# Kernel optimization log

Measured on AMD Instinct MI355X. Metric: run time of the kernel, lower is better.

## Reference

```python
import jax, jax.numpy as jnp
import numpy as np

B, T, D_LAT = 128, 256, 256
N_HIDDEN = 1024
H_SMALL = N_HIDDEN // 2  # 512: lstm1/lstm2 hidden size
H_BIG = N_HIDDEN         # 1024: lstm3 hidden size


def _p(key, shape, scale=0.05):
    return (jax.random.normal(key, shape, dtype=jnp.float32) * scale)


def setup_inputs() -> dict:
    key = jax.random.key(0)
    ks = jax.random.split(key, 16)
    return {
        "X": jax.random.normal(ks[0], (B, T, D_LAT), dtype=jnp.float32),
        # LSTMCell 1: input D_LAT -> hidden H_SMALL (torch layout: [4H, in])
        "W_ih1": _p(ks[1], (4 * H_SMALL, D_LAT)),
        "W_hh1": _p(ks[2], (4 * H_SMALL, H_SMALL)),
        "b_ih1": _p(ks[3], (4 * H_SMALL,)),
        "b_hh1": _p(ks[4], (4 * H_SMALL,)),
        # LSTMCell 2: H_SMALL -> H_SMALL
        "W_ih2": _p(ks[5], (4 * H_SMALL, H_SMALL)),
        "W_hh2": _p(ks[6], (4 * H_SMALL, H_SMALL)),
        "b_ih2": _p(ks[7], (4 * H_SMALL,)),
        "b_hh2": _p(ks[8], (4 * H_SMALL,)),
        # LSTMCell 3: H_SMALL -> H_BIG
        "W_ih3": _p(ks[9], (4 * H_BIG, H_SMALL)),
        "W_hh3": _p(ks[10], (4 * H_BIG, H_BIG)),
        "b_ih3": _p(ks[11], (4 * H_BIG,)),
        "b_hh3": _p(ks[12], (4 * H_BIG,)),
        # Linear: H_BIG -> D_LAT (torch layout: [out, in])
        "W_lin": _p(ks[13], (D_LAT, H_BIG)),
        "b_lin": _p(ks[14], (D_LAT,)),
    }


def _lstm_cell(x, h, c, W_ih, W_hh, b_ih, b_hh):
    # torch.nn.LSTMCell gate order: i, f, g, o
    gates = x @ W_ih.T + b_ih + h @ W_hh.T + b_hh  # [B, 4H]
    i, f, g, o = jnp.split(gates, 4, axis=-1)
    c_new = jax.nn.sigmoid(f) * c + jax.nn.sigmoid(i) * jnp.tanh(g)
    h_new = jax.nn.sigmoid(o) * jnp.tanh(c_new)
    return h_new, c_new


def reference(X, W_ih1, W_hh1, b_ih1, b_hh1,
              W_ih2, W_hh2, b_ih2, b_hh2,
              W_ih3, W_hh3, b_ih3, b_hh3,
              W_lin, b_lin):
    n = X.shape[0]
    z_s = jnp.zeros((n, H_SMALL), dtype=X.dtype)
    z_b = jnp.zeros((n, H_BIG), dtype=X.dtype)
    init = (z_s, z_s, z_s, z_s, z_b, z_b)

    def step(carry, x_t):
        h1, c1, h2, c2, h3, c3 = carry
        h1, c1 = _lstm_cell(x_t, h1, c1, W_ih1, W_hh1, b_ih1, b_hh1)
        h2, c2 = _lstm_cell(h1, h2, c2, W_ih2, W_hh2, b_ih2, b_hh2)
        h3, c3 = _lstm_cell(h2, h3, c3, W_ih3, W_hh3, b_ih3, b_hh3)
        out = h3 @ W_lin.T + b_lin  # [B, D_LAT]
        return (h1, c1, h2, c2, h3, c3), out

    xs = jnp.swapaxes(X, 0, 1)  # [T, B, D_LAT]
    _, outputs = jax.lax.scan(step, init, xs)
    return outputs  # [T, B, D_LAT] == torch.stack(outputs) with future=0
```

## Files before the change

### kernel.cpp

```cpp
#include <hip/hip_runtime.h>
#include <stdint.h>

#define NWG 208
#define NPHASE 259

typedef __attribute__((ext_vector_type(8))) short short8;
typedef __attribute__((ext_vector_type(4))) float floatx4;
typedef __attribute__((ext_vector_type(4))) unsigned int uintx4;

static constexpr int Bb = 128, Tt = 256, Dl = 256, Hs = 512, Hb = 1024;

static constexpr size_t OFF_FLAGS = 0;
static constexpr size_t OFF_B1  = 1024;
static constexpr size_t OFF_B2  = OFF_B1 + 2048*4;
static constexpr size_t OFF_B3  = OFF_B2 + 2048*4;
static constexpr size_t OFF_BL  = OFF_B3 + 4096*4;
static constexpr size_t OFF_W1  = OFF_BL + 1024;
static constexpr size_t OFF_W2  = OFF_W1 + (size_t)2048*768*2;
static constexpr size_t OFF_W3  = OFF_W2 + (size_t)2048*1024*2;
static constexpr size_t OFF_WL  = OFF_W3 + (size_t)4096*1536*2;
static constexpr size_t FIXED_END = OFF_WL + (size_t)256*1024*2;

template<int D> struct Lay {
  static constexpr size_t H1  = FIXED_END;
  static constexpr size_t H2  = H1 + (size_t)D*Bb*Hs*2;
  static constexpr size_t H3  = H2 + (size_t)D*Bb*Hs*2;
  static constexpr size_t XB  = H3 + (size_t)D*Bb*Hb*2;
  static constexpr size_t END = XB + (size_t)D*Bb*Dl*2;
};

static constexpr int SMEM_BYTES = 135168;
static constexpr int STG_OFF    = 131072;

__device__ __forceinline__ unsigned short f2bf(float f) {
  unsigned int u = __float_as_uint(f);
  unsigned int r = (u + 0x7fffu + ((u >> 16) & 1u)) >> 16;
  return (unsigned short)r;
}
__device__ __forceinline__ float sigm(float x) { return 1.f/(1.f + __expf(-x)); }
__device__ __forceinline__ float tanh_f(float x) {
  x = fminf(fmaxf(x, -15.f), 15.f);
  float e = __expf(-2.f*x);
  return (1.f - e)/(1.f + e);
}
__device__ __forceinline__ size_t blk_off(int row, int u) {
  return ((size_t)(u >> 5)*8 + (row >> 4))*512 + (size_t)((u & 31) >> 3)*128
       + (size_t)(row & 15)*8 + (u & 7);
}
__device__ __forceinline__ void st_dword_cg(void* p, unsigned int v) {
  asm volatile("global_store_dword %0, %1, off sc0 sc1" :: "v"(p), "v"(v) : "memory");
}
__device__ __forceinline__ void st_b128_cg(void* p, uintx4 v) {
  asm volatile("global_store_dwordx4 %0, %1, off sc0 sc1" :: "v"(p), "v"(v) : "memory");
}
__device__ __forceinline__ void waitcnt_vm0() {
  asm volatile("s_waitcnt vmcnt(0)" ::: "memory");
}

template<int D>
__global__ void lstm_init(
    const float* __restrict__ X,
    const float* __restrict__ Wih1, const float* __restrict__ Whh1,
    const float* __restrict__ bih1, const float* __restrict__ bhh1,
    const float* __restrict__ Wih2, const float* __restrict__ Whh2,
    const float* __restrict__ bih2, const float* __restrict__ bhh2,
    const float* __restrict__ Wih3, const float* __restrict__ Whh3,
    const float* __restrict__ bih3, const float* __restrict__ bhh3,
    const float* __restrict__ Wlin, const float* __restrict__ blin,
    unsigned char* __restrict__ ws)
{
  size_t i0 = (size_t)blockIdx.x*blockDim.x + threadIdx.x;
  size_t np = (size_t)gridDim.x*blockDim.x;

  unsigned int* fl = (unsigned int*)(ws + OFF_FLAGS);
  for (size_t i = i0; i < 256; i += np) fl[i] = (i < NWG) ? 0u : 0xFFFFFFFFu;

  float* b1 = (float*)(ws + OFF_B1);
  float* b2 = (float*)(ws + OFF_B2);
  float* b3 = (float*)(ws + OFF_B3);
  float* bl = (float*)(ws + OFF_BL);
  for (size_t i = i0; i < 2048; i += np) b1[i] = bih1[i] + bhh1[i];
  for (size_t i = i0; i < 2048; i += np) b2[i] = bih2[i] + bhh2[i];
  for (size_t i = i0; i < 4096; i += np) b3[i] = bih3[i] + bhh3[i];
  for (size_t i = i0; i < 256;  i += np) bl[i] = blin[i];

  unsigned short* w1 = (unsigned short*)(ws + OFF_W1);
  unsigned short* w2 = (unsigned short*)(ws + OFF_W2);
  unsigned short* w3 = (unsigned short*)(ws + OFF_W3);
  unsigned short* wl = (unsigned short*)(ws + OFF_WL);
  for (size_t i = i0; i < (size_t)2048*768; i += np) {
    size_t r = i/768, k = i - r*768;
    float v = (k < 256) ? Wih1[r*256 + k] : Whh1[r*512 + (k - 256)];
    w1[i] = f2bf(v);
  }
  for (size_t i = i0; i < (size_t)2048*1024; i += np) {
    size_t r = i >> 10, k = i & 1023;
    float v = (k < 512) ? Wih2[r*512 + k] : Whh2[r*512 + (k - 512)];
    w2[i] = f2bf(v);
  }
  for (size_t i = i0; i < (size_t)4096*1536; i += np) {
    size_t r = i/1536, k = i - r*1536;
    float v = (k < 512) ? Wih3[r*512 + k] : Whh3[r*1024 + (k - 512)];
    w3[i] = f2bf(v);
  }
  for (size_t i = i0; i < (size_t)256*1024; i += np) wl[i] = f2bf(Wlin[i]);

  unsigned short* rings = (unsigned short*)(ws + Lay<D>::H1);
  const size_t nring = (size_t)D*Bb*Hs + (size_t)D*Bb*Hs + (size_t)D*Bb*Hb;
  for (size_t i = i0; i < nring; i += np) rings[i] = 0;

  unsigned short* xb0 = (unsigned short*)(ws + Lay<D>::XB);
  for (size_t i = i0; i < (size_t)Bb*Dl; i += np) {
    size_t b = i >> 8, d = i & 255;
    xb0[blk_off((int)b, (int)d)] = f2bf(X[(b*(size_t)Tt + 0)*Dl + d]);
  }
}

template<int TYPE>
__device__ __forceinline__ void layer_phase(
    const unsigned short* __restrict__ segA,
    const unsigned short* __restrict__ segB,
    unsigned short* __restrict__ hout,
    unsigned char* __restrict__ smem,
    const float* __restrict__ bias_r,
    float (&creg)[2][2][4],
    int U0, int wv, int lane, int tid)
{
  constexpr int K    = (TYPE==0 ? 768 : TYPE==1 ? 1024 : 1536);
  constexpr int KB1  = (TYPE==0 ? 256 : 512);
  constexpr int MF   = (TYPE==2 ? 1 : 2);
  constexpr int CKS  = (TYPE==2 ? 8 : 4);
  constexpr int NCH  = K/(32*CKS);
  const int l15 = lane & 15;
  const int g   = l15 >> 2;
  const int mbase = (TYPE==2 ? wv*16 : (wv&3)*32);
  const int nfb   = (TYPE==2 ? 0 : (wv>>2)*2);

  const size_t lof = (size_t)(lane >> 4)*128 + (size_t)l15*8;
  const unsigned short* pa[MF];
  const unsigned short* pb[MF];
  #pragma unroll
  for (int mf = 0; mf < MF; ++mf) {
    const size_t rb = (size_t)((mbase >> 4) + mf)*512;
    pa[mf] = segA + rb + lof;
    pb[mf] = segB + rb + lof;
  }
  int rowbyte[2], xr[2];
  #pragma unroll
  for (int nf = 0; nf < 2; ++nf) {
    const int rp = (nfb + nf)*16 + l15;
    rowbyte[nf] = rp*(K*2);
    xr[nf] = (rp & 7) << 4;
  }
  const int klobyte = ((lane >> 4) << 3)*2;

  floatx4 acc[MF][2];
  #pragma unroll
  for (int mf = 0; mf < MF; ++mf)
    #pragma unroll
    for (int nf = 0; nf < 2; ++nf) {
      float bv = bias_r[nf];
      floatx4 b4 = {bv, bv, bv, bv};
      acc[mf][nf] = b4;
    }

  short8 A0[CKS][MF], A1[CKS][MF];
  auto LOADC = [&](int c, short8 (&A)[CKS][MF]) {
    #pragma unroll
    for (int ks = 0; ks < CKS; ++ks) {
      const int kb = (c*CKS + ks)*32;
      #pragma unroll
      for (int mf = 0; mf < MF; ++mf) {
        const unsigned short* p = (kb < KB1)
            ? pa[mf] + (size_t)(kb >> 5)*4096
            : pb[mf] + (size_t)((kb - KB1) >> 5)*4096;
        A[ks][mf] = *(const short8*)p;
      }
    }
  };
  auto MM = [&](int c, short8 (&A)[CKS][MF]) {
    #pragma unroll
    for (int ks = 0; ks < CKS; ++ks) {
      const int kb = (c*CKS + ks)*32;
      short8 bf[2];
      #pragma unroll
      for (int nf = 0; nf < 2; ++nf)
        bf[nf] = *(const short8*)(smem + rowbyte[nf] + ((kb*2 + klobyte) ^ xr[nf]));
      #pragma unroll
      for (int mf = 0; mf < MF; ++mf)
        #pragma unroll
        for (int nf = 0; nf < 2; ++nf)
          acc[mf][nf] = __builtin_amdgcn_mfma_f32_16x16x32_bf16(A[ks][mf], bf[nf], acc[mf][nf], 0, 0, 0);
    }
  };

  LOADC(0, A0);
  #pragma unroll 1
  for (int ch = 0; ch < NCH; ch += 2) {
    LOADC(ch + 1, A1);
    MM(ch, A0);
    if (ch + 2 < NCH) LOADC(ch + 2, A0);
    MM(ch + 1, A1);
  }

  unsigned short* stg = (unsigned short*)(smem + STG_OFF);
  const int a = (U0 & 31) >> 3;
  #pragma unroll
  for (int nf = 0; nf < 2; ++nf) {
    const int u = U0 + (nfb + nf)*4 + (l15 & 3);
    #pragma unroll
    for (int mf = 0; mf < MF; ++mf) {
      float h4[4];
      #pragma unroll
      for (int j = 0; j < 4; ++j) {
        float s0  = acc[mf][nf][j];
        float s4  = __shfl_xor(s0, 4);
        float s8  = __shfl_xor(s0, 8);
        float s12 = __shfl_xor(s0, 12);
        float iv = (g==0)?s0 :(g==1)?s4 :(g==2)?s8 :s12;
        float fv = (g==0)?s4 :(g==1)?s0 :(g==2)?s12:s8;
        float gv = (g==0)?s8 :(g==1)?s12:(g==2)?s0 :s4;
        float ov = (g==0)?s12:(g==1)?s8 :(g==2)?s4 :s0;
        float c  = sigm(fv)*creg[mf][nf][j] + sigm(iv)*tanh_f(gv);
        creg[mf][nf][j] = c;
        h4[j] = sigm(ov)*tanh_f(c);
      }
      float hs = (g==0)?h4[0]:(g==1)?h4[1]:(g==2)?h4[2]:h4[3];
      const int row = mbase + mf*16 + ((lane >> 4) << 2) + g;
      const int c2  = (TYPE==2) ? (row >> 4)
                                : ((row >> 4)*2 + (((u & 31) >> 3) - a));
      stg[c2*128 + (row & 15)*8 + (u & 7)] = f2bf(hs);
    }
  }
  __syncthreads();

  const size_t gbase = (size_t)(U0 >> 5)*4096;
  if (TYPE == 2) {
    if (tid < 128) {
      const int c2 = tid >> 4, w = tid & 15;
      short8 v = *(const short8*)(stg + c2*128 + w*8);
      st_b128_cg(hout + gbase + (size_t)c2*512 + (size_t)a*128 + w*8, *(uintx4*)&v);
    }
  } else {
    if (tid < 256) {
      const int c2 = tid >> 4, w = tid & 15;
      short8 v = *(const short8*)(stg + c2*128 + w*8);
      st_b128_cg(hout + gbase + (size_t)(c2 >> 1)*512 + (size_t)(a + (c2 & 1))*128 + w*8, *(uintx4*)&v);
    }
  }
}

template<int D>
__global__ void __launch_bounds__(512, 2)
lstm_persist(const float* __restrict__ X, float* __restrict__ out,
             unsigned char* __restrict__ ws)
{
  extern __shared__ unsigned char smem[];

  __builtin_amdgcn_fence(__ATOMIC_ACQUIRE, "agent");

  const int tid  = threadIdx.x;
  const int lane = tid & 63;
  const int wv   = tid >> 6;
  const int wg   = blockIdx.x;
  const int l15  = lane & 15;

  unsigned int* flags = (unsigned int*)(ws + OFF_FLAGS);
  const float* bias1 = (const float*)(ws + OFF_B1);
  const float* bias2 = (const float*)(ws + OFF_B2);
  const float* bias3 = (const float*)(ws + OFF_B3);
  const float* biasl = (const float*)(ws + OFF_BL);
  const unsigned short* W1 = (const unsigned short*)(ws + OFF_W1);
  const unsigned short* W2 = (const unsigned short*)(ws + OFF_W2);
  const unsigned short* W3 = (const unsigned short*)(ws + OFF_W3);
  const unsigned short* WL = (const unsigned short*)(ws + OFF_WL);
  unsigned short* h1r = (unsigned short*)(ws + Lay<D>::H1);
  unsigned short* h2r = (unsigned short*)(ws + Lay<D>::H2);
  unsigned short* h3r = (unsigned short*)(ws + Lay<D>::H3);
  unsigned short* Xb  = (unsigned short*)(ws + Lay<D>::XB);

  auto slot = [](int t) -> size_t { return (size_t)(t & (D - 1)); };
  const size_t HSs = (size_t)Bb*Hs, HBs = (size_t)Bb*Hb, XBs = (size_t)Bb*Dl;

  int type, U0 = 0, osec = 0, K = 0, WROWS = 0, HGATE = 0;
  const unsigned short* Wg = nullptr; const float* biasp = nullptr;
  if (wg < 32)        { type = 0; U0 = wg*16;        Wg = W1; biasp = bias1; K = 768;  WROWS = 64; HGATE = 512; }
  else if (wg < 64)   { type = 1; U0 = (wg-32)*16;   Wg = W2; biasp = bias2; K = 1024; WROWS = 64; HGATE = 512; }
  else if (wg < 192)  { type = 2; U0 = (wg-64)*8;    Wg = W3; biasp = bias3; K = 1536; WROWS = 32; HGATE = 1024; }
  else                { type = 3; osec = (wg-192)*16; Wg = WL; K = 1024; WROWS = 16; }

  {
    const int rowchunks = K >> 3;
    for (int idx = tid; idx < WROWS*rowchunks; idx += 512) {
      const int rp = idx / rowchunks, kc = idx - rp*rowchunks;
      int R;
      if (type == 3) R = osec + rp;
      else {
        const int c = rp & 15;
        R = (c >> 2)*HGATE + U0 + (rp >> 4)*4 + (c & 3);
      }
      uintx4 v = *(const uintx4*)(Wg + (size_t)R*K + kc*8);
      const int db = rp*(K*2) + ((kc*16) ^ ((rp & 7) << 4));
      *(uintx4*)(smem + db) = v;
    }
  }

  float bias_r[2] = {0.f, 0.f};
  if (type < 3) {
    const int g   = l15 >> 2;
    const int nfb = (type == 2 ? 0 : (wv >> 2)*2);
    #pragma unroll
    for (int nf = 0; nf < 2; ++nf) {
      const int u = U0 + (nfb + nf)*4 + (l15 & 3);
      bias_r[nf] = biasp[g*HGATE + u];
    }
  } else {
    bias_r[0] = biasl[osec + l15];
  }

  float creg[2][2][4];
  #pragma unroll
  for (int a = 0; a < 2; ++a)
    #pragma unroll
    for (int b = 0; b < 2; ++b)
      #pragma unroll
      for (int c = 0; c < 4; ++c) creg[a][b][c] = 0.f;

  __syncthreads();

  for (int p = 0; p < NPHASE; ++p) {
    if (type == 0) {
      const int t = p;
      if (t < Tt)
        layer_phase<0>(Xb + slot(t)*XBs,
                       h1r + slot(t-1)*HSs,
                       h1r + slot(t)*HSs,
                       smem, bias_r, creg, U0, wv, lane, tid);
    } else if (type == 1) {
      const int t = p - 1;
      if (t >= 0 && t < Tt)
        layer_phase<1>(h1r + slot(t)*HSs,
                       h2r + slot(t-1)*HSs,
                       h2r + slot(t)*HSs,
                       smem, bias_r, creg, U0, wv, lane, tid);
    } else if (type == 2) {
      const int t = p - 2;
      if (t >= 0 && t < Tt)
        layer_phase<2>(h2r + slot(t)*HSs,
                       h3r + slot(t-1)*HBs,
                       h3r + slot(t)*HBs,
                       smem, bias_r, creg, U0, wv, lane, tid);
    } else {
      if (p + 1 < Tt && tid < 256) {
        const int tx = p + 1;
        const int j = wg - 192;
        const int i = tid*8;
        const int row = j*8 + (i >> 8);
        const int d = i & 255;
        const float* xp = X + ((size_t)row*Tt + tx)*Dl + d;
        float4 f0 = *(const float4*)xp;
        float4 f1 = *(const float4*)(xp + 4);
        uintx4 pk;
        pk[0] = (unsigned int)f2bf(f0.x) | ((unsigned int)f2bf(f0.y) << 16);
        pk[1] = (unsigned int)f2bf(f0.z) | ((unsigned int)f2bf(f0.w) << 16);
        pk[2] = (unsigned int)f2bf(f1.x) | ((unsigned int)f2bf(f1.y) << 16);
        pk[3] = (unsigned int)f2bf(f1.z) | ((unsigned int)f2bf(f1.w) << 16);
        st_b128_cg(Xb + slot(tx)*XBs + blk_off(row, d), pk);
      }
      const int to = p - 3;
      if (to >= 0 && to < Tt) {
        const unsigned short* hA = h3r + slot(to)*HBs;
        const size_t lof = (size_t)(lane >> 4)*128 + (size_t)l15*8;
        const unsigned short* pa0 = hA + (size_t)wv*512 + lof;
        const int rowbyte = l15*2048;
        const int xr = (l15 & 7) << 4;
        const int klobyte = ((lane >> 4) << 3)*2;
        floatx4 oacc;
        { floatx4 b4 = {bias_r[0], bias_r[0], bias_r[0], bias_r[0]}; oacc = b4; }
        short8 A0[4], A1[4];
        auto HLOAD = [&](int c, short8 (&A)[4]) {
          #pragma unroll
          for (int ks = 0; ks < 4; ++ks)
            A[ks] = *(const short8*)(pa0 + (size_t)(c*4 + ks)*4096);
        };
        auto HMM = [&](int c, short8 (&A)[4]) {
          #pragma unroll
          for (int ks = 0; ks < 4; ++ks) {
            const int kb = c*128 + ks*32;
            short8 bw = *(const short8*)(smem + rowbyte + ((kb*2 + klobyte) ^ xr));
            oacc = __builtin_amdgcn_mfma_f32_16x16x32_bf16(A[ks], bw, oacc, 0, 0, 0);
          }
        };
        HLOAD(0, A0);
        #pragma unroll 1
        for (int ch = 0; ch < 8; ch += 2) {
          HLOAD(ch + 1, A1);
          HMM(ch, A0);
          if (ch + 2 < 8) HLOAD(ch + 2, A0);
          HMM(ch + 1, A1);
        }
        const int col = osec + l15;
        const int b0 = wv*16 + ((lane >> 4) << 2);
        #pragma unroll
        for (int j = 0; j < 4; ++j)
          st_dword_cg(out + ((size_t)to*Bb + b0 + j)*Dl + col,
                      __float_as_uint(oacc[j]));
      }
    }

    if (p < NPHASE - 1) {
      waitcnt_vm0();
      __syncthreads();
      const unsigned int tgt = (unsigned int)(p + 1);
      if (tid == 0) st_dword_cg(flags + wg, tgt);
      if (tid < 64) {
        uintx4 f;
        for (;;) {
          asm volatile("global_load_dwordx4 %0, %1, off sc0 sc1\n\t"
                       "s_waitcnt vmcnt(0)"
                       : "=v"(f) : "v"(flags + lane*4) : "memory");
          if (f[0] >= tgt && f[1] >= tgt && f[2] >= tgt && f[3] >= tgt) break;
          __builtin_amdgcn_s_sleep(4);
        }
      }
      __syncthreads();
      if (D == 2 || (p & 7) == 7)
        __builtin_amdgcn_fence(__ATOMIC_ACQUIRE, "agent");
    }
  }
}

extern "C" void kernel_launch(void* const* d_in, const int* in_sizes, int n_in,
                              void* d_out, int out_size, void* d_ws, size_t ws_size,
                              hipStream_t stream)
{
  const float* X    = (const float*)d_in[0];
  const float* Wih1 = (const float*)d_in[1];
  const float* Whh1 = (const float*)d_in[2];
  const float* bih1 = (const float*)d_in[3];
  const float* bhh1 = (const float*)d_in[4];
  const float* Wih2 = (const float*)d_in[5];
  const float* Whh2 = (const float*)d_in[6];
  const float* bih2 = (const float*)d_in[7];
  const float* bhh2 = (const float*)d_in[8];
  const float* Wih3 = (const float*)d_in[9];
  const float* Whh3 = (const float*)d_in[10];
  const float* bih3 = (const float*)d_in[11];
  const float* bhh3 = (const float*)d_in[12];
  const float* Wlin = (const float*)d_in[13];
  const float* blin = (const float*)d_in[14];
  unsigned char* ws = (unsigned char*)d_ws;

  if (ws_size >= Lay<8>::END) {
    lstm_init<8><<<2048, 256, 0, stream>>>(X, Wih1, Whh1, bih1, bhh1,
                                           Wih2, Whh2, bih2, bhh2,
                                           Wih3, Whh3, bih3, bhh3,
                                           Wlin, blin, ws);
    lstm_persist<8><<<NWG, 512, SMEM_BYTES, stream>>>(X, (float*)d_out, ws);
  } else if (ws_size >= Lay<2>::END) {
    lstm_init<2><<<2048, 256, 0, stream>>>(X, Wih1, Whh1, bih1, bhh1,
                                           Wih2, Whh2, bih2, bhh2,
                                           Wih3, Whh3, bih3, bhh3,
                                           Wlin, blin, ws);
    lstm_persist<2><<<NWG, 512, SMEM_BYTES, stream>>>(X, (float*)d_out, ws);
  }
}
```

Measured before the change: 3.812 ms.

## Replace global phase barrier with per-layer dataflow flags and deeper ring buffers

Drops the lockstep all-workgroup barrier per phase. Each layer group now waits only on the flags of its producers (previous layer at t, itself at t-1) and its ring-buffer consumers (about 31 steps back), so layers can pipeline freely with up to 32 slots of slack. All of X is converted to bf16 in the init kernel instead of being staged per step by the output workgroups. This removes global barrier stalls at the cost of more workspace and more flag polling per wait. If the workspace is too small the launch now returns without computing anything.

```diff
diff --git a/kernel.cpp b/kernel.cpp
--- a/kernel.cpp
+++ b/kernel.cpp
@@ -2,13 +2,13 @@
 #include <stdint.h>
 
 #define NWG 208
-#define NPHASE 259
 
 typedef __attribute__((ext_vector_type(8))) short short8;
 typedef __attribute__((ext_vector_type(4))) float floatx4;
 typedef __attribute__((ext_vector_type(4))) unsigned int uintx4;
 
 static constexpr int Bb = 128, Tt = 256, Dl = 256, Hs = 512, Hb = 1024;
+static constexpr int D = 32;
 
 static constexpr size_t OFF_FLAGS = 0;
 static constexpr size_t OFF_B1  = 1024;
@@ -20,14 +20,11 @@
 static constexpr size_t OFF_W3  = OFF_W2 + (size_t)2048*1024*2;
 static constexpr size_t OFF_WL  = OFF_W3 + (size_t)4096*1536*2;
 static constexpr size_t FIXED_END = OFF_WL + (size_t)256*1024*2;
-
-template<int D> struct Lay {
-  static constexpr size_t H1  = FIXED_END;
-  static constexpr size_t H2  = H1 + (size_t)D*Bb*Hs*2;
-  static constexpr size_t H3  = H2 + (size_t)D*Bb*Hs*2;
-  static constexpr size_t XB  = H3 + (size_t)D*Bb*Hb*2;
-  static constexpr size_t END = XB + (size_t)D*Bb*Dl*2;
-};
+static constexpr size_t OFF_H1R  = FIXED_END;
+static constexpr size_t OFF_H2R  = OFF_H1R + (size_t)D*Bb*Hs*2;
+static constexpr size_t OFF_H3R  = OFF_H2R + (size_t)D*Bb*Hs*2;
+static constexpr size_t OFF_XALL = OFF_H3R + (size_t)D*Bb*Hb*2;
+static constexpr size_t WS_NEED  = OFF_XALL + (size_t)Tt*Bb*Dl*2;
 
 static constexpr int SMEM_BYTES = 135168;
 static constexpr int STG_OFF    = 131072;
@@ -57,7 +54,21 @@
   asm volatile("s_waitcnt vmcnt(0)" ::: "memory");
 }
 
-template<int D>
+__device__ __forceinline__ void wait_ge(const unsigned int* f, int n, int tgt, int lane) {
+  if (tgt <= 0) return;
+  for (;;) {
+    int ok = 1;
+    for (int i = lane; i < n; i += 64) {
+      unsigned v;
+      asm volatile("global_load_dword %0, %1, off sc0 sc1\n\ts_waitcnt vmcnt(0)"
+                   : "=v"(v) : "v"(f + i) : "memory");
+      if ((int)v < tgt) ok = 0;
+    }
+    if (__all(ok)) return;
+    __builtin_amdgcn_s_sleep(2);
+  }
+}
+
 __global__ void lstm_init(
     const float* __restrict__ X,
     const float* __restrict__ Wih1, const float* __restrict__ Whh1,
@@ -73,7 +84,7 @@
   size_t np = (size_t)gridDim.x*blockDim.x;
 
   unsigned int* fl = (unsigned int*)(ws + OFF_FLAGS);
-  for (size_t i = i0; i < 256; i += np) fl[i] = (i < NWG) ? 0u : 0xFFFFFFFFu;
+  for (size_t i = i0; i < 256; i += np) fl[i] = 0u;
 
   float* b1 = (float*)(ws + OFF_B1);
   float* b2 = (float*)(ws + OFF_B2);
@@ -105,14 +116,15 @@
   }
   for (size_t i = i0; i < (size_t)256*1024; i += np) wl[i] = f2bf(Wlin[i]);
 
-  unsigned short* rings = (unsigned short*)(ws + Lay<D>::H1);
+  unsigned short* rings = (unsigned short*)(ws + OFF_H1R);
   const size_t nring = (size_t)D*Bb*Hs + (size_t)D*Bb*Hs + (size_t)D*Bb*Hb;
   for (size_t i = i0; i < nring; i += np) rings[i] = 0;
 
-  unsigned short* xb0 = (unsigned short*)(ws + Lay<D>::XB);
-  for (size_t i = i0; i < (size_t)Bb*Dl; i += np) {
-    size_t b = i >> 8, d = i & 255;
-    xb0[blk_off((int)b, (int)d)] = f2bf(X[(b*(size_t)Tt + 0)*Dl + d]);
+  unsigned short* xall = (unsigned short*)(ws + OFF_XALL);
+  for (size_t i = i0; i < (size_t)Tt*Bb*Dl; i += np) {
+    size_t t = i >> 15, rem = i & 32767;
+    size_t b = rem >> 8, d = rem & 255;
+    xall[t*32768 + blk_off((int)b, (int)d)] = f2bf(X[(b*(size_t)Tt + t)*Dl + d]);
   }
 }
 
@@ -250,10 +262,8 @@
   }
 }
 
-template<int D>
 __global__ void __launch_bounds__(512, 2)
-lstm_persist(const float* __restrict__ X, float* __restrict__ out,
-             unsigned char* __restrict__ ws)
+lstm_persist(float* __restrict__ out, unsigned char* __restrict__ ws)
 {
   extern __shared__ unsigned char smem[];
 
@@ -274,10 +284,10 @@
   const unsigned short* W2 = (const unsigned short*)(ws + OFF_W2);
   const unsigned short* W3 = (const unsigned short*)(ws + OFF_W3);
   const unsigned short* WL = (const unsigned short*)(ws + OFF_WL);
-  unsigned short* h1r = (unsigned short*)(ws + Lay<D>::H1);
-  unsigned short* h2r = (unsigned short*)(ws + Lay<D>::H2);
-  unsigned short* h3r = (unsigned short*)(ws + Lay<D>::H3);
-  unsigned short* Xb  = (unsigned short*)(ws + Lay<D>::XB);
+  unsigned short* h1r = (unsigned short*)(ws + OFF_H1R);
+  unsigned short* h2r = (unsigned short*)(ws + OFF_H2R);
+  unsigned short* h3r = (unsigned short*)(ws + OFF_H3R);
+  unsigned short* Xall = (unsigned short*)(ws + OFF_XALL);
 
   auto slot = [](int t) -> size_t { return (size_t)(t & (D - 1)); };
   const size_t HSs = (size_t)Bb*Hs, HBs = (size_t)Bb*Hb, XBs = (size_t)Bb*Dl;
@@ -328,105 +338,79 @@
 
   __syncthreads();
 
-  for (int p = 0; p < NPHASE; ++p) {
+  for (int t = 0; t < Tt; ++t) {
+    if (wv == 0) {
+      if (type == 0)      { wait_ge(flags + 0, 32, t, lane);
+                            wait_ge(flags + 32, 32, t - 31, lane); }
+      else if (type == 1) { wait_ge(flags + 0, 32, t + 1, lane);
+                            wait_ge(flags + 32, 32, t, lane);
+                            wait_ge(flags + 64, 128, t - 31, lane); }
+      else if (type == 2) { wait_ge(flags + 32, 32, t + 1, lane);
+                            wait_ge(flags + 64, 128, t, lane);
+                            wait_ge(flags + 192, 16, t - 31, lane); }
+      else                { wait_ge(flags + 64, 128, t + 1, lane); }
+    }
+    __syncthreads();
+
     if (type == 0) {
-      const int t = p;
-      if (t < Tt)
-        layer_phase<0>(Xb + slot(t)*XBs,
-                       h1r + slot(t-1)*HSs,
-                       h1r + slot(t)*HSs,
-                       smem, bias_r, creg, U0, wv, lane, tid);
+      layer_phase<0>(Xall + (size_t)t*XBs,
+                     h1r + slot(t-1)*HSs,
+                     h1r + slot(t)*HSs,
+                     smem, bias_r, creg, U0, wv, lane, tid);
     } else if (type == 1) {
-      const int t = p - 1;
-      if (t >= 0 && t < Tt)
-        layer_phase<1>(h1r + slot(t)*HSs,
-                       h2r + slot(t-1)*HSs,
-                       h2r + slot(t)*HSs,
-                       smem, bias_r, creg, U0, wv, lane, tid);
+      layer_phase<1>(h1r + slot(t)*HSs,
+                     h2r + slot(t-1)*HSs,
+                     h2r + slot(t)*HSs,
+                     smem, bias_r, creg, U0, wv, lane, tid);
     } else if (type == 2) {
-      const int t = p - 2;
-      if (t >= 0 && t < Tt)
-        layer_phase<2>(h2r + slot(t)*HSs,
-                       h3r + slot(t-1)*HBs,
-                       h3r + slot(t)*HBs,
-                       smem, bias_r, creg, U0, wv, lane, tid);
+      layer_phase<2>(h2r + slot(t)*HSs,
+                     h3r + slot(t-1)*HBs,
+                     h3r + slot(t)*HBs,
+                     smem, bias_r, creg, U0, wv, lane, tid);
     } else {
-      if (p + 1 < Tt && tid < 256) {
-        const int tx = p + 1;
-        const int j = wg - 192;
-        const int i = tid*8;
-        const int row = j*8 + (i >> 8);
-        const int d = i & 255;
-        const float* xp = X + ((size_t)row*Tt + tx)*Dl + d;
-        float4 f0 = *(const float4*)xp;
-        float4 f1 = *(const float4*)(xp + 4);
-        uintx4 pk;
-        pk[0] = (unsigned int)f2bf(f0.x) | ((unsigned int)f2bf(f0.y) << 16);
-        pk[1] = (unsigned int)f2bf(f0.z) | ((unsigned int)f2bf(f0.w) << 16);
-        pk[2] = (unsigned int)f2bf(f1.x) | ((unsigned int)f2bf(f1.y) << 16);
-        pk[3] = (unsigned int)f2bf(f1.z) | ((unsigned int)f2bf(f1.w) << 16);
-        st_b128_cg(Xb + slot(tx)*XBs + blk_off(row, d), pk);
+      const unsigned short* hA = h3r + slot(t)*HBs;
+      const size_t lof = (size_t)(lane >> 4)*128 + (size_t)l15*8;
+      const unsigned short* pa0 = hA + (size_t)wv*512 + lof;
+      const int rowbyte = l15*2048;
+      const int xr = (l15 & 7) << 4;
+      const int klobyte = ((lane >> 4) << 3)*2;
+      floatx4 oacc;
+      { floatx4 b4 = {bias_r[0], bias_r[0], bias_r[0], bias_r[0]}; oacc = b4; }
+      short8 A0[4], A1[4];
+      auto HLOAD = [&](int c, short8 (&A)[4]) {
+        #pragma unroll
+        for (int ks = 0; ks < 4; ++ks)
+          A[ks] = *(const short8*)(pa0 + (size_t)(c*4 + ks)*4096);
+      };
+      auto HMM = [&](int c, short8 (&A)[4]) {
+        #pragma unroll
+        for (int ks = 0; ks < 4; ++ks) {
+          const int kb = c*128 + ks*32;
+          short8 bw = *(const short8*)(smem + rowbyte + ((kb*2 + klobyte) ^ xr));
+          oacc = __builtin_amdgcn_mfma_f32_16x16x32_bf16(A[ks], bw, oacc, 0, 0, 0);
+        }
+      };
+      HLOAD(0, A0);
+      #pragma unroll 1
+      for (int ch = 0; ch < 8; ch += 2) {
+        HLOAD(ch + 1, A1);
+        HMM(ch, A0);
+        if (ch + 2 < 8) HLOAD(ch + 2, A0);
+        HMM(ch + 1, A1);
       }
-      const int to = p - 3;
-      if (to >= 0 && to < Tt) {
-        const unsigned short* hA = h3r + slot(to)*HBs;
-        const size_t lof = (size_t)(lane >> 4)*128 + (size_t)l15*8;
-        const unsigned short* pa0 = hA + (size_t)wv*512 + lof;
-        const int rowbyte = l15*2048;
-        const int xr = (l15 & 7) << 4;
-        const int klobyte = ((lane >> 4) << 3)*2;
-        floatx4 oacc;
-        { floatx4 b4 = {bias_r[0], bias_r[0], bias_r[0], bias_r[0]}; oacc = b4; }
-        short8 A0[4], A1[4];
-        auto HLOAD = [&](int c, short8 (&A)[4]) {
-          #pragma unroll
-          for (int ks = 0; ks < 4; ++ks)
-            A[ks] = *(const short8*)(pa0 + (size_t)(c*4 + ks)*4096);
-        };
-        auto HMM = [&](int c, short8 (&A)[4]) {
-          #pragma unroll
-          for (int ks = 0; ks < 4; ++ks) {
-            const int kb = c*128 + ks*32;
-            short8 bw = *(const short8*)(smem + rowbyte + ((kb*2 + klobyte) ^ xr));
-            oacc = __builtin_amdgcn_mfma_f32_16x16x32_bf16(A[ks], bw, oacc, 0, 0, 0);
-          }
-        };
-        HLOAD(0, A0);
-        #pragma unroll 1
-        for (int ch = 0; ch < 8; ch += 2) {
-          HLOAD(ch + 1, A1);
-          HMM(ch, A0);
-          if (ch + 2 < 8) HLOAD(ch + 2, A0);
-          HMM(ch + 1, A1);
-        }
-        const int col = osec + l15;
-        const int b0 = wv*16 + ((lane >> 4) << 2);
-        #pragma unroll
-        for (int j = 0; j < 4; ++j)
-          st_dword_cg(out + ((size_t)to*Bb + b0 + j)*Dl + col,
-                      __float_as_uint(oacc[j]));
-      }
-    }
-
-    if (p < NPHASE - 1) {
-      waitcnt_vm0();
-      __syncthreads();
-      const unsigned int tgt = (unsigned int)(p + 1);
-      if (tid == 0) st_dword_cg(flags + wg, tgt);
-      if (tid < 64) {
-        uintx4 f;
-        for (;;) {
-          asm volatile("global_load_dwordx4 %0, %1, off sc0 sc1\n\t"
-                       "s_waitcnt vmcnt(0)"
-                       : "=v"(f) : "v"(flags + lane*4) : "memory");
-          if (f[0] >= tgt && f[1] >= tgt && f[2] >= tgt && f[3] >= tgt) break;
-          __builtin_amdgcn_s_sleep(4);
-        }
-      }
-      __syncthreads();
-      if (D == 2 || (p & 7) == 7)
-        __builtin_amdgcn_fence(__ATOMIC_ACQUIRE, "agent");
-    }
+      const int col = osec + l15;
+      const int b0 = wv*16 + ((lane >> 4) << 2);
+      #pragma unroll
+      for (int j = 0; j < 4; ++j)
+        st_dword_cg(out + ((size_t)t*Bb + b0 + j)*Dl + col,
+                    __float_as_uint(oacc[j]));
+    }
+
+    waitcnt_vm0();
+    __syncthreads();
+    if (tid == 0) st_dword_cg(flags + wg, (unsigned)(t + 1));
+    if ((t & 7) == 7)
+      __builtin_amdgcn_fence(__ATOMIC_ACQUIRE, "agent");
   }
 }
 
@@ -434,6 +418,8 @@
                               void* d_out, int out_size, void* d_ws, size_t ws_size,
                               hipStream_t stream)
 {
+  if (ws_size < WS_NEED) return;
+
   const float* X    = (const float*)d_in[0];
   const float* Wih1 = (const float*)d_in[1];
   const float* Whh1 = (const float*)d_in[2];
@@ -451,17 +437,9 @@
   const float* blin = (const float*)d_in[14];
   unsigned char* ws = (unsigned char*)d_ws;
 
-  if (ws_size >= Lay<8>::END) {
-    lstm_init<8><<<2048, 256, 0, stream>>>(X, Wih1, Whh1, bih1, bhh1,
-                                           Wih2, Whh2, bih2, bhh2,
-                                           Wih3, Whh3, bih3, bhh3,
-                                           Wlin, blin, ws);
-    lstm_persist<8><<<NWG, 512, SMEM_BYTES, stream>>>(X, (float*)d_out, ws);
-  } else if (ws_size >= Lay<2>::END) {
-    lstm_init<2><<<2048, 256, 0, stream>>>(X, Wih1, Whh1, bih1, bhh1,
-                                           Wih2, Whh2, bih2, bhh2,
-                                           Wih3, Whh3, bih3, bhh3,
-                                           Wlin, blin, ws);
-    lstm_persist<2><<<NWG, 512, SMEM_BYTES, stream>>>(X, (float*)d_out, ws);
-  }
-}
+  lstm_init<<<2048, 256, 0, stream>>>(X, Wih1, Whh1, bih1, bhh1,
+                                      Wih2, Whh2, bih2, bhh2,
+                                      Wih3, Whh3, bih3, bhh3,
+                                      Wlin, blin, ws);
+  lstm_persist<<<NWG, 512, SMEM_BYTES, stream>>>((float*)d_out, ws);
+}
```

Measured after the change: 3.470 ms. 9.0% less time.
